# Kernel optimization log

Measured on AMD Instinct MI355X. Metric: run time of the kernel, lower is better.

Reference implementation:

```python
import jax, jax.numpy as jnp
from jax import lax
import numpy as np

B, C, H, W = 2, 256, 256, 256
NH, P = 8, 4
D = C // NH
EPS_BN = 1e-5
EPS_LN = 1e-5
EPS_ATT = 1e-6


def _maxpool(t):
    return lax.reduce_window(t, -jnp.inf, lax.max, (1, 1, P, P), (1, 1, P, P), 'VALID')


def _ln(t, g, b):  # t: [..., C]
    m = t.mean(-1, keepdims=True)
    v = ((t - m) ** 2).mean(-1, keepdims=True)
    return (t - m) * jax.lax.rsqrt(v + EPS_LN) * g + b


def _dw_bn(t, w, g, b, mu, var):  # depthwise 3x3 conv + BatchNorm2d (eval)
    y = lax.conv_general_dilated(t, w, (1, 1), ((1, 1), (1, 1)),
                                 dimension_numbers=('NCHW', 'OIHW', 'NCHW'),
                                 feature_group_count=C)
    s = g * jax.lax.rsqrt(var + EPS_BN)
    return y * s[None, :, None, None] + (b - mu * s)[None, :, None, None]


def _tokens(t, h, w):  # [N,(NH D),h,w] -> [N,(h w),NH,D]
    return t.reshape(-1, NH, D, h, w).transpose(0, 3, 4, 1, 2).reshape(-1, h * w, NH, D)


def setup_inputs() -> dict:
    key = jax.random.key(0)
    ks = jax.random.split(key, 16)
    inp = {
        'x': jax.random.normal(ks[0], (B, C, H, W), jnp.float32),
        'source': jax.random.normal(ks[1], (B, C, H, W), jnp.float32),
        'ln1_g': jnp.ones((C,), jnp.float32),
        'ln1_b': jnp.zeros((C,), jnp.float32),
        'merge_w': jax.random.normal(ks[2], (C, C), jnp.float32) * (1.0 / np.sqrt(C)),
        'mlp_w1': jax.random.normal(ks[3], (2 * C, 2 * C), jnp.float32) * (1.0 / np.sqrt(2 * C)),
        'mlp_w2': jax.random.normal(ks[4], (C, 2 * C), jnp.float32) * (1.0 / np.sqrt(2 * C)),
        'ln2_g': jnp.ones((C,), jnp.float32),
        'ln2_b': jnp.zeros((C,), jnp.float32),
    }
    for i, p in enumerate(['q', 'k', 'v']):
        kk = jax.random.split(ks[5 + i], 3)
        inp[p + '_w'] = jax.random.normal(kk[0], (C, 1, 3, 3), jnp.float32) * 0.2
        inp[p + '_bn_g'] = jnp.ones((C,), jnp.float32)
        inp[p + '_bn_b'] = jnp.zeros((C,), jnp.float32)
        inp[p + '_bn_m'] = jax.random.normal(kk[1], (C,), jnp.float32) * 0.05
        inp[p + '_bn_v'] = jax.random.uniform(kk[2], (C,), jnp.float32, 0.5, 1.5)
    return inp


def _forward(x, source, ln1_g, ln1_b,
             q_w, q_bn_g, q_bn_b, q_bn_m, q_bn_v,
             k_w, k_bn_g, k_bn_b, k_bn_m, k_bn_v,
             v_w, v_bn_g, v_bn_b, v_bn_m, v_bn_v,
             merge_w, mlp_w1, mlp_w2, ln2_g, ln2_b):
    h, w = H // P, W // P
    L = h * w
    # pre-norm after pooling (norm_before=True, max_pool path)
    q_sp = _ln(_maxpool(x).transpose(0, 2, 3, 1), ln1_g, ln1_b).transpose(0, 3, 1, 2)
    s_sp = _ln(_maxpool(source).transpose(0, 2, 3, 1), ln1_g, ln1_b).transpose(0, 3, 1, 2)
    # conv QKV projections (depthwise 3x3 + BN)
    q = _tokens(_dw_bn(q_sp, q_w, q_bn_g, q_bn_b, q_bn_m, q_bn_v), h, w)
    k = _tokens(_dw_bn(s_sp, k_w, k_bn_g, k_bn_b, k_bn_m, k_bn_v), h, w)
    v = _tokens(_dw_bn(s_sp, v_w, v_bn_g, v_bn_b, v_bn_m, v_bn_v), h, w)
    # LoFTR LinearAttention: feature map elu(x)+1
    Q = jax.nn.elu(q) + 1.0
    K = jax.nn.elu(k) + 1.0
    v_len = v.shape[1]
    KV = jnp.einsum('nshd,nshv->nhdv', K, v / v_len)
    Z = 1.0 / (jnp.einsum('nlhd,nhd->nlh', Q, K.sum(axis=1)) + EPS_ATT)
    msg = jnp.einsum('nlhd,nhdv,nlh->nlhv', Q, KV, Z) * v_len  # [N,L,NH,D]
    # merge + upsample
    msg = msg.reshape(B, L, C) @ merge_w.T
    msg = msg.reshape(B, h, w, C).transpose(0, 3, 1, 2)
    msg = jax.image.resize(msg, (B, C, H, W), method='bilinear')
    # merge-MLP + norm2 + residual
    cat = jnp.concatenate([x, msg], axis=1).transpose(0, 2, 3, 1)  # [B,H,W,2C]
    m = jax.nn.relu(cat @ mlp_w1.T) @ mlp_w2.T
    m = _ln(m, ln2_g, ln2_b).transpose(0, 3, 1, 2)
    return x + m


def reference(x, source, ln1_g, ln1_b,
              q_w, q_bn_g, q_bn_b, q_bn_m, q_bn_v,
              k_w, k_bn_g, k_bn_b, k_bn_m, k_bn_v,
              v_w, v_bn_g, v_bn_b, v_bn_m, v_bn_v,
              merge_w, mlp_w1, mlp_w2, ln2_g, ln2_b):
    return _forward(x, source, ln1_g, ln1_b,
                    q_w, q_bn_g, q_bn_b, q_bn_m, q_bn_v,
                    k_w, k_bn_g, k_bn_b, k_bn_m, k_bn_v,
                    v_w, v_bn_g, v_bn_b, v_bn_m, v_bn_v,
                    merge_w, mlp_w1, mlp_w2, ln2_g, ln2_b)
```

## Files before the change

kernel.cpp:

```cpp
#include <hip/hip_runtime.h>
#include <hip/hip_bf16.h>
#include <cstdint>


typedef __attribute__((ext_vector_type(8))) short bf16x8;
typedef __attribute__((ext_vector_type(4))) float f32x4;

#define SWZ(p, off) ((off) ^ (((p) & 7) << 4))

__device__ inline unsigned pk2bf(float a, float b) {
    unsigned ua = __builtin_bit_cast(unsigned, a);
    ua += 0x7fffu + ((ua >> 16) & 1u);
    unsigned ub = __builtin_bit_cast(unsigned, b);
    ub += 0x7fffu + ((ub >> 16) & 1u);
    return (ua >> 16) | (ub & 0xffff0000u);
}
__device__ inline float bitf(unsigned u) { return __builtin_bit_cast(float, u); }

__global__ void build_wimg(const float* __restrict__ w1, const float* __restrict__ w2,
                           uint4* __restrict__ w1img, uint4* __restrict__ w2img) {
    int idx = blockIdx.x * 256 + threadIdx.x;
    if (idx < 32768) {
        int rk = idx >> 11, jt = (idx >> 6) & 31, l = idx & 63;
        int j = jt * 16 + (l & 15);
        int k0 = rk * 32 + 8 * (l >> 4);
        const float* s = w1 + j * 512 + k0;
        uint4 pk;
        pk.x = pk2bf(s[0], s[1]); pk.y = pk2bf(s[2], s[3]);
        pk.z = pk2bf(s[4], s[5]); pk.w = pk2bf(s[6], s[7]);
        w1img[idx] = pk;
    } else {
        int id2 = idx - 32768;
        int rj = id2 >> 10, ct = (id2 >> 6) & 15, l = id2 & 63;
        int c = ct * 16 + (l & 15);
        int j0 = rj * 32 + 8 * (l >> 4);
        const float* s = w2 + c * 512 + j0;
        uint4 pk;
        pk.x = pk2bf(s[0], s[1]); pk.y = pk2bf(s[2], s[3]);
        pk.z = pk2bf(s[4], s[5]); pk.w = pk2bf(s[6], s[7]);
        w2img[id2] = pk;
    }
}

__global__ __launch_bounds__(512) void poolln_k(
    const float* __restrict__ x, const float* __restrict__ src,
    const float* __restrict__ g, const float* __restrict__ bvec,
    float* __restrict__ q_sp, float* __restrict__ s_sp) {
    __shared__ __align__(16) float tile[16640];
    __shared__ float ps[512];
    __shared__ float pq[512];
    __shared__ float mr[64];
    __shared__ float rr[64];
    int qy = blockIdx.x, b = blockIdx.y, z = blockIdx.z;
    const float* in = z ? src : x;
    float* out = z ? s_sp : q_sp;
    int t = threadIdx.x;
    int qx = t & 63;
    int gq = t >> 6;
    for (int cc = 0; cc < 32; cc++) {
        int cl = gq + cc * 8;
        const float* rp = in + (((b * 256 + cl) * 256) + 4 * qy) * 256 + 4 * qx;
        float4 r0 = *(const float4*)(rp);
        float4 r1 = *(const float4*)(rp + 256);
        float4 r2 = *(const float4*)(rp + 512);
        float4 r3 = *(const float4*)(rp + 768);
        float m = fmaxf(fmaxf(fmaxf(r0.x, r0.y), fmaxf(r0.z, r0.w)),
                        fmaxf(fmaxf(r1.x, r1.y), fmaxf(r1.z, r1.w)));
        m = fmaxf(m, fmaxf(fmaxf(r2.x, r2.y), fmaxf(r2.z, r2.w)));
        m = fmaxf(m, fmaxf(fmaxf(r3.x, r3.y), fmaxf(r3.z, r3.w)));
        tile[cl * 65 + qx] = m;
    }
    __syncthreads();
    {
        float s = 0.f, q = 0.f;
        for (int i = 0; i < 32; i++) {
            float v = tile[(gq * 32 + i) * 65 + qx];
            s += v; q += v * v;
        }
        ps[gq * 64 + qx] = s;
        pq[gq * 64 + qx] = q;
    }
    __syncthreads();
    if (t < 64) {
        float s = 0.f, q = 0.f;
#pragma unroll
        for (int ww = 0; ww < 8; ww++) { s += ps[ww * 64 + t]; q += pq[ww * 64 + t]; }
        float mean = s * (1.f / 256.f);
        float var = q * (1.f / 256.f) - mean * mean;
        mr[t] = mean; rr[t] = rsqrtf(var + 1e-5f);
    }
    __syncthreads();
    for (int cb4 = 0; cb4 < 4; cb4++) {
#pragma unroll
        for (int kk = 0; kk < 8; kk++) {
            int cl = t & 63;
            int qxx = gq + kk * 8;
            int c = cb4 * 64 + cl;
            float v = tile[c * 65 + qxx];
            out[((b * 64 + qy) * 64 + qxx) * 256 + c] =
                (v - mr[qxx]) * rr[qxx] * g[c] + bvec[c];
        }
    }
}

__global__ void dwconv_k(const float* __restrict__ q_sp, const float* __restrict__ s_sp,
                         const float* __restrict__ qw, const float* __restrict__ qg,
                         const float* __restrict__ qb, const float* __restrict__ qm,
                         const float* __restrict__ qvar,
                         const float* __restrict__ kw, const float* __restrict__ kg,
                         const float* __restrict__ kb, const float* __restrict__ km,
                         const float* __restrict__ kvar,
                         const float* __restrict__ vw, const float* __restrict__ vg,
                         const float* __restrict__ vb, const float* __restrict__ vm,
                         const float* __restrict__ vvar,
                         float* __restrict__ qf, float* __restrict__ kf, float* __restrict__ vf) {
    int bid = blockIdx.x;
    int b = bid >> 12, l = bid & 4095, y = l >> 6, xx = l & 63;
    int c = threadIdx.x;
    float aq = 0.f, ak = 0.f, av = 0.f;
#pragma unroll
    for (int ky = 0; ky < 3; ky++) {
        int yy = y + ky - 1;
        if (yy < 0 || yy > 63) continue;
#pragma unroll
        for (int kx = 0; kx < 3; kx++) {
            int x2 = xx + kx - 1;
            if (x2 < 0 || x2 > 63) continue;
            int off = ((b * 64 + yy) * 64 + x2) * 256 + c;
            float a = q_sp[off], s = s_sp[off];
            aq += a * qw[c * 9 + ky * 3 + kx];
            ak += s * kw[c * 9 + ky * 3 + kx];
            av += s * vw[c * 9 + ky * 3 + kx];
        }
    }
    float sq = qg[c] * rsqrtf(qvar[c] + 1e-5f);
    float sk = kg[c] * rsqrtf(kvar[c] + 1e-5f);
    float sv = vg[c] * rsqrtf(vvar[c] + 1e-5f);
    float oq = aq * sq + (qb[c] - qm[c] * sq);
    float ok = ak * sk + (kb[c] - km[c] * sk);
    float ov = av * sv + (vb[c] - vm[c] * sv);
    oq = oq > 0.f ? oq + 1.f : expm1f(oq) + 1.f;
    ok = ok > 0.f ? ok + 1.f : expm1f(ok) + 1.f;
    int o = (b * 4096 + l) * 256 + c;
    qf[o] = oq; kf[o] = ok; vf[o] = ov;
}

__global__ void kv_part(const float* __restrict__ kf, const float* __restrict__ vf,
                        float* __restrict__ kvp, float* __restrict__ kspart) {
    __shared__ float red[4][1024];
    __shared__ float kred[4][32];
    int bid = blockIdx.x;
    int bnh = bid >> 4, ch = bid & 15;
    int b = bnh >> 3, nh = bnh & 7;
    int t = threadIdx.x;
    int ls = t >> 6, dkg = (t >> 3) & 7, dvg = t & 7;
    const float* kb = kf + (size_t)b * 4096 * 256 + nh * 32 + dkg * 4;
    const float* vb = vf + (size_t)b * 4096 * 256 + nh * 32 + dvg * 4;
    int l0 = ch * 256 + ls * 64;
    float4 a0 = {0,0,0,0}, a1 = a0, a2 = a0, a3 = a0, ks = a0;
    for (int l = l0; l < l0 + 64; l++) {
        float4 k4 = *(const float4*)(kb + (size_t)l * 256);
        float4 v4 = *(const float4*)(vb + (size_t)l * 256);
        a0.x += k4.x * v4.x; a0.y += k4.x * v4.y; a0.z += k4.x * v4.z; a0.w += k4.x * v4.w;
        a1.x += k4.y * v4.x; a1.y += k4.y * v4.y; a1.z += k4.y * v4.z; a1.w += k4.y * v4.w;
        a2.x += k4.z * v4.x; a2.y += k4.z * v4.y; a2.z += k4.z * v4.z; a2.w += k4.z * v4.w;
        a3.x += k4.w * v4.x; a3.y += k4.w * v4.y; a3.z += k4.w * v4.z; a3.w += k4.w * v4.w;
        ks.x += k4.x; ks.y += k4.y; ks.z += k4.z; ks.w += k4.w;
    }
    int base = dkg * 128 + dvg * 4;
    *(float4*)(&red[ls][base])      = a0;
    *(float4*)(&red[ls][base + 32]) = a1;
    *(float4*)(&red[ls][base + 64]) = a2;
    *(float4*)(&red[ls][base + 96]) = a3;
    if (dvg == 0) *(float4*)(&kred[ls][dkg * 4]) = ks;
    __syncthreads();
    for (int e = t; e < 1024; e += 256)
        kvp[bid * 1024 + e] = red[0][e] + red[1][e] + red[2][e] + red[3][e];
    if (t < 32) kspart[bid * 32 + t] = kred[0][t] + kred[1][t] + kred[2][t] + kred[3][t];
}

__global__ void kv_red(const float* __restrict__ kvp, const float* __restrict__ kspart,
                       float* __restrict__ kv, float* __restrict__ ksum) {
    int bnh = blockIdx.x;
    int t = threadIdx.x;
    for (int e = t; e < 1024; e += 256) {
        float s = 0.f;
        for (int ch = 0; ch < 16; ch++) s += kvp[(bnh * 16 + ch) * 1024 + e];
        kv[bnh * 1024 + e] = s;
    }
    if (t < 32) {
        float s = 0.f;
        for (int ch = 0; ch < 16; ch++) s += kspart[(bnh * 16 + ch) * 32 + t];
        ksum[bnh * 32 + t] = s;
    }
}

__global__ void msgmerge_k(const float* __restrict__ qf, const float* __restrict__ kv,
                           const float* __restrict__ ksum, const float* __restrict__ mw,
                           float* __restrict__ merged) {
    __shared__ float Qs[8 * 256];
    __shared__ float Ms[8 * 256];
    int bid = blockIdx.x;
    int b = bid >> 9, l0 = (bid & 511) * 8;
    int t = threadIdx.x;
#pragma unroll
    for (int tt = 0; tt < 8; tt++) Qs[tt * 256 + t] = qf[(b * 4096 + l0 + tt) * 256 + t];
    __syncthreads();
    int nh = t >> 5, dv = t & 31;
    const float* kvb = kv + (b * 8 + nh) * 1024 + dv;
    const float* ksb = ksum + (b * 8 + nh) * 32;
    float sacc[8] = {0, 0, 0, 0, 0, 0, 0, 0};
    float zacc[8] = {0, 0, 0, 0, 0, 0, 0, 0};
    for (int dk = 0; dk < 32; dk++) {
        float kvv = kvb[dk * 32];
        float ksv = ksb[dk];
#pragma unroll
        for (int tt = 0; tt < 8; tt++) {
            float qv = Qs[tt * 256 + nh * 32 + dk];
            sacc[tt] += qv * kvv;
            zacc[tt] += qv * ksv;
        }
    }
#pragma unroll
    for (int tt = 0; tt < 8; tt++) Ms[tt * 256 + t] = sacc[tt] / (zacc[tt] + 1e-6f);
    __syncthreads();
    float acc8[8] = {0, 0, 0, 0, 0, 0, 0, 0};
    const float* wrow = mw + t * 256;
    for (int c = 0; c < 256; c++) {
        float wv = wrow[c];
#pragma unroll
        for (int tt = 0; tt < 8; tt++) acc8[tt] += Ms[tt * 256 + c] * wv;
    }
#pragma unroll
    for (int tt = 0; tt < 8; tt++) merged[(b * 4096 + l0 + tt) * 256 + t] = acc8[tt];
}

__global__ __launch_bounds__(1024) __attribute__((amdgpu_waves_per_eu(4))) void mlp_k(
    const float* __restrict__ x, const float* __restrict__ merged,
    const uint4* __restrict__ w1img, const uint4* __restrict__ w2img,
    const float* __restrict__ g2, const float* __restrict__ b2,
    float* __restrict__ out) {
    __shared__ __align__(16) char CATB[65536];
    __shared__ float ps[1024];
    __shared__ float pq[1024];
    __shared__ float mr[64];
    __shared__ float rr[64];
    __shared__ char lds_pad[12288];
    const int t = threadIdx.x;
    const int lane = t & 63;
    const int l15 = lane & 15, l4 = lane >> 4;
    const int w = t >> 6;
    const int X0 = blockIdx.x * 64;
    const int Y = blockIdx.y;
    const int b = blockIdx.z;
    if (g2 == nullptr) lds_pad[t] = 1;

    {
        const int p = lane;
        const int cg = w;
#pragma unroll
        for (int it = 0; it < 2; it++) {
            int c0 = cg * 16 + it * 8;
            float v[8];
#pragma unroll
            for (int j = 0; j < 8; j++)
                v[j] = x[((b * 256 + c0 + j) * 256 + Y) * 256 + X0 + p];
            uint4 pk;
            pk.x = pk2bf(v[0], v[1]); pk.y = pk2bf(v[2], v[3]);
            pk.z = pk2bf(v[4], v[5]); pk.w = pk2bf(v[6], v[7]);
            *(uint4*)(CATB + SWZ(p, p * 1024 + c0 * 2)) = pk;
        }
        float sy = (Y - 1.5f) * 0.25f;
        int iy0 = (int)floorf(sy);
        float fy = sy - (float)iy0;
        int y0c = iy0 < 0 ? 0 : iy0;
        int y1c = (iy0 + 1) > 63 ? 63 : (iy0 + 1);
        int X = X0 + p;
        float sx = (X - 1.5f) * 0.25f;
        int ix0 = (int)floorf(sx);
        float fx = sx - (float)ix0;
        int x0c = ix0 < 0 ? 0 : ix0;
        int x1c = (ix0 + 1) > 63 ? 63 : (ix0 + 1);
        float w00 = (1.f - fy) * (1.f - fx), w01 = (1.f - fy) * fx;
        float w10 = fy * (1.f - fx), w11 = fy * fx;
        const float* m00 = merged + ((b * 64 + y0c) * 64 + x0c) * 256;
        const float* m01 = merged + ((b * 64 + y0c) * 64 + x1c) * 256;
        const float* m10 = merged + ((b * 64 + y1c) * 64 + x0c) * 256;
        const float* m11 = merged + ((b * 64 + y1c) * 64 + x1c) * 256;
#pragma unroll
        for (int it = 0; it < 2; it++) {
            int c0 = cg * 16 + it * 8;
            float v[8];
#pragma unroll
            for (int j = 0; j < 8; j++)
                v[j] = w00 * m00[c0 + j] + w01 * m01[c0 + j] + w10 * m10[c0 + j] + w11 * m11[c0 + j];
            uint4 pk;
            pk.x = pk2bf(v[0], v[1]); pk.y = pk2bf(v[2], v[3]);
            pk.z = pk2bf(v[4], v[5]); pk.w = pk2bf(v[6], v[7]);
            *(uint4*)(CATB + SWZ(p, p * 1024 + (256 + c0) * 2)) = pk;
        }
    }
    __syncthreads();

    f32x4 acc[2][4];
#pragma unroll
    for (int a = 0; a < 2; a++)
#pragma unroll
        for (int n = 0; n < 4; n++) acc[a][n] = (f32x4){0.f, 0.f, 0.f, 0.f};
    {
        const uint4* w1p = w1img + (w * 2) * 64 + lane;
        for (int rk = 0; rk < 16; rk++) {
            bf16x8 wa[2];
#pragma unroll
            for (int a = 0; a < 2; a++) wa[a] = *(const bf16x8*)(w1p + rk * 2048 + a * 64);
#pragma unroll
            for (int n = 0; n < 4; n++) {
                int pr = n * 16 + l15;
                bf16x8 bfr = *(const bf16x8*)(CATB + SWZ(pr, pr * 1024 + rk * 64 + l4 * 16));
#pragma unroll
                for (int a = 0; a < 2; a++)
                    acc[a][n] = __builtin_amdgcn_mfma_f32_16x16x32_bf16(wa[a], bfr, acc[a][n], 0, 0, 0);
            }
        }
    }

    uint2 xs[4];
    {
        int c0 = w * 16 + l4 * 4;
#pragma unroll
        for (int n = 0; n < 4; n++) {
            int px = n * 16 + l15;
            xs[n] = *(const uint2*)(CATB + SWZ(px, px * 1024 + c0 * 2));
        }
    }
    __syncthreads();

#pragma unroll
    for (int a = 0; a < 2; a++) {
        int j0 = w * 32 + a * 16 + l4 * 4;
#pragma unroll
        for (int n = 0; n < 4; n++) {
            int pr = n * 16 + l15;
            uint2 u;
            u.x = pk2bf(fmaxf(acc[a][n][0], 0.f), fmaxf(acc[a][n][1], 0.f));
            u.y = pk2bf(fmaxf(acc[a][n][2], 0.f), fmaxf(acc[a][n][3], 0.f));
            *(uint2*)(CATB + SWZ(pr, pr * 1024 + j0 * 2)) = u;
        }
    }
    __syncthreads();

    f32x4 macc[4];
#pragma unroll
    for (int n = 0; n < 4; n++) macc[n] = (f32x4){0.f, 0.f, 0.f, 0.f};
    {
        const uint4* w2p = w2img + w * 64 + lane;
        for (int rj = 0; rj < 16; rj++) {
            bf16x8 va = *(const bf16x8*)(w2p + rj * 1024);
#pragma unroll
            for (int n = 0; n < 4; n++) {
                int pr = n * 16 + l15;
                bf16x8 bfr = *(const bf16x8*)(CATB + SWZ(pr, pr * 1024 + rj * 64 + l4 * 16));
                macc[n] = __builtin_amdgcn_mfma_f32_16x16x32_bf16(va, bfr, macc[n], 0, 0, 0);
            }
        }
    }

#pragma unroll
    for (int n = 0; n < 4; n++) {
        float ss = 0.f, qq = 0.f;
#pragma unroll
        for (int r = 0; r < 4; r++) { float vv = macc[n][r]; ss += vv; qq += vv * vv; }
        ss += __shfl_xor(ss, 16); ss += __shfl_xor(ss, 32);
        qq += __shfl_xor(qq, 16); qq += __shfl_xor(qq, 32);
        if (l4 == 0) {
            ps[w * 64 + n * 16 + l15] = ss;
            pq[w * 64 + n * 16 + l15] = qq;
        }
    }
    __syncthreads();
    if (t < 64) {
        float ss = 0.f, qq = 0.f;
#pragma unroll
        for (int ww = 0; ww < 16; ww++) {
            ss += ps[ww * 64 + t];
            qq += pq[ww * 64 + t];
        }
        float mean = ss * (1.f / 256.f);
        float var = qq * (1.f / 256.f) - mean * mean;
        mr[t] = mean; rr[t] = rsqrtf(var + 1e-5f);
    }
    __syncthreads();
    {
        int cbase = w * 16 + l4 * 4;
        float gg[4], bb[4];
#pragma unroll
        for (int r = 0; r < 4; r++) { gg[r] = g2[cbase + r]; bb[r] = b2[cbase + r]; }
#pragma unroll
        for (int n = 0; n < 4; n++) {
            int px = n * 16 + l15;
            uint2 u = xs[n];
            float xr[4];
            xr[0] = bitf(u.x << 16); xr[1] = bitf(u.x & 0xffff0000u);
            xr[2] = bitf(u.y << 16); xr[3] = bitf(u.y & 0xffff0000u);
            float mean = mr[px], rs = rr[px];
#pragma unroll
            for (int r = 0; r < 4; r++) {
                out[((b * 256 + cbase + r) * 256 + Y) * 256 + X0 + px] =
                    xr[r] + (macc[n][r] - mean) * rs * gg[r] + bb[r];
            }
        }
    }
}

extern "C" void kernel_launch(void* const* d_in, const int* in_sizes, int n_in,
                              void* d_out, int out_size, void* d_ws, size_t ws_size,
                              hipStream_t stream) {
    const float* x       = (const float*)d_in[0];
    const float* source  = (const float*)d_in[1];
    const float* ln1_g   = (const float*)d_in[2];
    const float* ln1_b   = (const float*)d_in[3];
    const float* merge_w = (const float*)d_in[4];
    const float* mlp_w1  = (const float*)d_in[5];
    const float* mlp_w2  = (const float*)d_in[6];
    const float* ln2_g   = (const float*)d_in[7];
    const float* ln2_b   = (const float*)d_in[8];
    const float* q_w = (const float*)d_in[9];
    const float* q_bn_g = (const float*)d_in[10];
    const float* q_bn_b = (const float*)d_in[11];
    const float* q_bn_m = (const float*)d_in[12];
    const float* q_bn_v = (const float*)d_in[13];
    const float* k_w = (const float*)d_in[14];
    const float* k_bn_g = (const float*)d_in[15];
    const float* k_bn_b = (const float*)d_in[16];
    const float* k_bn_m = (const float*)d_in[17];
    const float* k_bn_v = (const float*)d_in[18];
    const float* v_w = (const float*)d_in[19];
    const float* v_bn_g = (const float*)d_in[20];
    const float* v_bn_b = (const float*)d_in[21];
    const float* v_bn_m = (const float*)d_in[22];
    const float* v_bn_v = (const float*)d_in[23];
    float* out = (float*)d_out;

    float* ws = (float*)d_ws;
    float* q_sp   = ws + 0;
    float* s_sp   = ws + 2097152;
    float* qf     = ws + 4194304;
    float* kf     = ws + 6291456;
    float* vf     = ws + 8388608;
    float* merged = ws + 10485760;
    float* kvp    = ws + 0;
    float* kspart = ws + 262144;
    float* kv     = ws + 12650496;
    float* ksum   = ws + 12666880;
    uint4* w1img  = (uint4*)((char*)d_ws + 50669568);
    uint4* w2img  = (uint4*)((char*)d_ws + 51193856);

    build_wimg<<<192, 256, 0, stream>>>(mlp_w1, mlp_w2, w1img, w2img);
    poolln_k<<<dim3(64, 2, 2), 512, 0, stream>>>(x, source, ln1_g, ln1_b, q_sp, s_sp);
    dwconv_k<<<8192, 256, 0, stream>>>(q_sp, s_sp,
                                       q_w, q_bn_g, q_bn_b, q_bn_m, q_bn_v,
                                       k_w, k_bn_g, k_bn_b, k_bn_m, k_bn_v,
                                       v_w, v_bn_g, v_bn_b, v_bn_m, v_bn_v,
                                       qf, kf, vf);
    kv_part<<<256, 256, 0, stream>>>(kf, vf, kvp, kspart);
    kv_red<<<16, 256, 0, stream>>>(kvp, kspart, kv, ksum);
    msgmerge_k<<<1024, 256, 0, stream>>>(qf, kv, ksum, merge_w, merged);
    mlp_k<<<dim3(4, 256, 2), 1024, 0, stream>>>(x, merged, w1img, w2img, ln2_g, ln2_b, out);
}
```

Before: 336.5 us.

## Halve MLP block to 512 threads with larger per-wave MFMA tiles

The fused MLP kernel now runs 8 waves per block instead of 16. Each wave computes twice as many output rows, so every LDS B-fragment read feeds 4 (first GEMM) or 2 (second GEMM) MFMAs, which cuts LDS traffic per MFMA. The LDS padding array that capped occupancy is removed. The residual now rereads x from global memory in fp32 instead of keeping a bf16 copy in registers, which also changes numerics slightly. The cost is more accumulator registers per thread and fewer waves to hide latency.

```diff
diff --git a/kernel.cpp b/kernel.cpp
--- a/kernel.cpp
+++ b/kernel.cpp
@@ -235,17 +235,16 @@
     for (int tt = 0; tt < 8; tt++) merged[(b * 4096 + l0 + tt) * 256 + t] = acc8[tt];
 }
 
-__global__ __launch_bounds__(1024) __attribute__((amdgpu_waves_per_eu(4))) void mlp_k(
+__global__ __launch_bounds__(512) __attribute__((amdgpu_waves_per_eu(4))) void mlp_k(
     const float* __restrict__ x, const float* __restrict__ merged,
     const uint4* __restrict__ w1img, const uint4* __restrict__ w2img,
     const float* __restrict__ g2, const float* __restrict__ b2,
     float* __restrict__ out) {
     __shared__ __align__(16) char CATB[65536];
-    __shared__ float ps[1024];
-    __shared__ float pq[1024];
+    __shared__ float ps[512];
+    __shared__ float pq[512];
     __shared__ float mr[64];
     __shared__ float rr[64];
-    __shared__ char lds_pad[12288];
     const int t = threadIdx.x;
     const int lane = t & 63;
     const int l15 = lane & 15, l4 = lane >> 4;
@@ -253,14 +252,12 @@
     const int X0 = blockIdx.x * 64;
     const int Y = blockIdx.y;
     const int b = blockIdx.z;
-    if (g2 == nullptr) lds_pad[t] = 1;
 
     {
         const int p = lane;
-        const int cg = w;
-#pragma unroll
-        for (int it = 0; it < 2; it++) {
-            int c0 = cg * 16 + it * 8;
+#pragma unroll
+        for (int it = 0; it < 4; it++) {
+            int c0 = w * 32 + it * 8;
             float v[8];
 #pragma unroll
             for (int j = 0; j < 8; j++)
@@ -288,8 +285,8 @@
         const float* m10 = merged + ((b * 64 + y1c) * 64 + x0c) * 256;
         const float* m11 = merged + ((b * 64 + y1c) * 64 + x1c) * 256;
 #pragma unroll
-        for (int it = 0; it < 2; it++) {
-            int c0 = cg * 16 + it * 8;
+        for (int it = 0; it < 4; it++) {
+            int c0 = w * 32 + it * 8;
             float v[8];
 #pragma unroll
             for (int j = 0; j < 8; j++)
@@ -302,42 +299,34 @@
     }
     __syncthreads();
 
-    f32x4 acc[2][4];
-#pragma unroll
-    for (int a = 0; a < 2; a++)
+    f32x4 acc[4][4];
+#pragma unroll
+    for (int a = 0; a < 4; a++)
 #pragma unroll
         for (int n = 0; n < 4; n++) acc[a][n] = (f32x4){0.f, 0.f, 0.f, 0.f};
     {
-        const uint4* w1p = w1img + (w * 2) * 64 + lane;
+        const uint4* w1p = w1img + (w * 4) * 64 + lane;
         for (int rk = 0; rk < 16; rk++) {
-            bf16x8 wa[2];
-#pragma unroll
-            for (int a = 0; a < 2; a++) wa[a] = *(const bf16x8*)(w1p + rk * 2048 + a * 64);
+            bf16x8 bf[4];
 #pragma unroll
             for (int n = 0; n < 4; n++) {
                 int pr = n * 16 + l15;
-                bf16x8 bfr = *(const bf16x8*)(CATB + SWZ(pr, pr * 1024 + rk * 64 + l4 * 16));
-#pragma unroll
-                for (int a = 0; a < 2; a++)
-                    acc[a][n] = __builtin_amdgcn_mfma_f32_16x16x32_bf16(wa[a], bfr, acc[a][n], 0, 0, 0);
+                bf[n] = *(const bf16x8*)(CATB + SWZ(pr, pr * 1024 + rk * 64 + l4 * 16));
             }
-        }
-    }
-
-    uint2 xs[4];
-    {
-        int c0 = w * 16 + l4 * 4;
-#pragma unroll
-        for (int n = 0; n < 4; n++) {
-            int px = n * 16 + l15;
-            xs[n] = *(const uint2*)(CATB + SWZ(px, px * 1024 + c0 * 2));
-        }
-    }
-    __syncthreads();
-
-#pragma unroll
-    for (int a = 0; a < 2; a++) {
-        int j0 = w * 32 + a * 16 + l4 * 4;
+#pragma unroll
+            for (int a = 0; a < 4; a++) {
+                bf16x8 wa = *(const bf16x8*)(w1p + rk * 2048 + a * 64);
+#pragma unroll
+                for (int n = 0; n < 4; n++)
+                    acc[a][n] = __builtin_amdgcn_mfma_f32_16x16x32_bf16(wa, bf[n], acc[a][n], 0, 0, 0);
+            }
+        }
+    }
+    __syncthreads();
+
+#pragma unroll
+    for (int a = 0; a < 4; a++) {
+        int j0 = w * 64 + a * 16 + l4 * 4;
 #pragma unroll
         for (int n = 0; n < 4; n++) {
             int pr = n * 16 + l15;
@@ -349,18 +338,26 @@
     }
     __syncthreads();
 
-    f32x4 macc[4];
-#pragma unroll
-    for (int n = 0; n < 4; n++) macc[n] = (f32x4){0.f, 0.f, 0.f, 0.f};
+    f32x4 macc[2][4];
+#pragma unroll
+    for (int c = 0; c < 2; c++)
+#pragma unroll
+        for (int n = 0; n < 4; n++) macc[c][n] = (f32x4){0.f, 0.f, 0.f, 0.f};
     {
-        const uint4* w2p = w2img + w * 64 + lane;
+        const uint4* w2p = w2img + (w * 2) * 64 + lane;
         for (int rj = 0; rj < 16; rj++) {
-            bf16x8 va = *(const bf16x8*)(w2p + rj * 1024);
+            bf16x8 bf[4];
 #pragma unroll
             for (int n = 0; n < 4; n++) {
                 int pr = n * 16 + l15;
-                bf16x8 bfr = *(const bf16x8*)(CATB + SWZ(pr, pr * 1024 + rj * 64 + l4 * 16));
-                macc[n] = __builtin_amdgcn_mfma_f32_16x16x32_bf16(va, bfr, macc[n], 0, 0, 0);
+                bf[n] = *(const bf16x8*)(CATB + SWZ(pr, pr * 1024 + rj * 64 + l4 * 16));
+            }
+#pragma unroll
+            for (int c = 0; c < 2; c++) {
+                bf16x8 va = *(const bf16x8*)(w2p + rj * 1024 + c * 64);
+#pragma unroll
+                for (int n = 0; n < 4; n++)
+                    macc[c][n] = __builtin_amdgcn_mfma_f32_16x16x32_bf16(va, bf[n], macc[c][n], 0, 0, 0);
             }
         }
     }
@@ -369,7 +366,9 @@
     for (int n = 0; n < 4; n++) {
         float ss = 0.f, qq = 0.f;
 #pragma unroll
-        for (int r = 0; r < 4; r++) { float vv = macc[n][r]; ss += vv; qq += vv * vv; }
+        for (int c = 0; c < 2; c++)
+#pragma unroll
+            for (int r = 0; r < 4; r++) { float vv = macc[c][n][r]; ss += vv; qq += vv * vv; }
         ss += __shfl_xor(ss, 16); ss += __shfl_xor(ss, 32);
         qq += __shfl_xor(qq, 16); qq += __shfl_xor(qq, 32);
         if (l4 == 0) {
@@ -381,7 +380,7 @@
     if (t < 64) {
         float ss = 0.f, qq = 0.f;
 #pragma unroll
-        for (int ww = 0; ww < 16; ww++) {
+        for (int ww = 0; ww < 8; ww++) {
             ss += ps[ww * 64 + t];
             qq += pq[ww * 64 + t];
         }
@@ -390,23 +389,20 @@
         mr[t] = mean; rr[t] = rsqrtf(var + 1e-5f);
     }
     __syncthreads();
-    {
-        int cbase = w * 16 + l4 * 4;
+#pragma unroll
+    for (int cc = 0; cc < 2; cc++) {
+        int cbase = w * 32 + cc * 16 + l4 * 4;
         float gg[4], bb[4];
 #pragma unroll
         for (int r = 0; r < 4; r++) { gg[r] = g2[cbase + r]; bb[r] = b2[cbase + r]; }
 #pragma unroll
         for (int n = 0; n < 4; n++) {
             int px = n * 16 + l15;
-            uint2 u = xs[n];
-            float xr[4];
-            xr[0] = bitf(u.x << 16); xr[1] = bitf(u.x & 0xffff0000u);
-            xr[2] = bitf(u.y << 16); xr[3] = bitf(u.y & 0xffff0000u);
             float mean = mr[px], rs = rr[px];
 #pragma unroll
             for (int r = 0; r < 4; r++) {
-                out[((b * 256 + cbase + r) * 256 + Y) * 256 + X0 + px] =
-                    xr[r] + (macc[n][r] - mean) * rs * gg[r] + bb[r];
+                int off = ((b * 256 + cbase + r) * 256 + Y) * 256 + X0 + px;
+                out[off] = x[off] + (macc[cc][n][r] - mean) * rs * gg[r] + bb[r];
             }
         }
     }
@@ -465,5 +461,5 @@
     kv_part<<<256, 256, 0, stream>>>(kf, vf, kvp, kspart);
     kv_red<<<16, 256, 0, stream>>>(kvp, kspart, kv, ksum);
     msgmerge_k<<<1024, 256, 0, stream>>>(qf, kv, ksum, merge_w, merged);
-    mlp_k<<<dim3(4, 256, 2), 1024, 0, stream>>>(x, merged, w1img, w2img, ln2_g, ln2_b, out);
-}
+    mlp_k<<<dim3(4, 256, 2), 512, 0, stream>>>(x, merged, w1img, w2img, ln2_g, ln2_b, out);
+}
```

Measured after the change: 404.9 us. 1.2x slower.

## Double-buffer MLP weight tiles in LDS via global_load_lds

Applied to the files above, without the earlier changes.

The mlp_k kernel now copies each k-slice of the packed W1 and W2 weight images into a double-buffered LDS area (WBUF) with direct global-to-LDS loads, prefetching slice k+1 while computing on slice k. MFMA operands are then read from LDS instead of from per-wave global loads. This is meant to hide global/L2 latency on the weight stream. In exchange it adds a block-wide barrier every iteration of both GEMM loops and grows LDS use past the old padding. It also relies on the barrier covering completion of the asynchronous LDS DMA.

```diff
diff --git a/kernel.cpp b/kernel.cpp
--- a/kernel.cpp
+++ b/kernel.cpp
@@ -16,6 +16,12 @@
     return (ua >> 16) | (ub & 0xffff0000u);
 }
 __device__ inline float bitf(unsigned u) { return __builtin_bit_cast(float, u); }
+
+__device__ inline void gl_lds16(const void* g, void* l) {
+    __builtin_amdgcn_global_load_lds(
+        (const __attribute__((address_space(1))) void*)g,
+        (__attribute__((address_space(3))) void*)l, 16, 0, 0);
+}
 
 __global__ void build_wimg(const float* __restrict__ w1, const float* __restrict__ w2,
                            uint4* __restrict__ w1img, uint4* __restrict__ w2img) {
@@ -241,11 +247,11 @@
     const float* __restrict__ g2, const float* __restrict__ b2,
     float* __restrict__ out) {
     __shared__ __align__(16) char CATB[65536];
+    __shared__ __align__(16) uint4 WBUF[4096];
     __shared__ float ps[1024];
     __shared__ float pq[1024];
     __shared__ float mr[64];
     __shared__ float rr[64];
-    __shared__ char lds_pad[12288];
     const int t = threadIdx.x;
     const int lane = t & 63;
     const int l15 = lane & 15, l4 = lane >> 4;
@@ -253,7 +259,9 @@
     const int X0 = blockIdx.x * 64;
     const int Y = blockIdx.y;
     const int b = blockIdx.z;
-    if (g2 == nullptr) lds_pad[t] = 1;
+
+    gl_lds16(w1img + t, WBUF + t);
+    gl_lds16(w1img + 1024 + t, WBUF + 1024 + t);
 
     {
         const int p = lane;
@@ -307,21 +315,28 @@
     for (int a = 0; a < 2; a++)
 #pragma unroll
         for (int n = 0; n < 4; n++) acc[a][n] = (f32x4){0.f, 0.f, 0.f, 0.f};
-    {
-        const uint4* w1p = w1img + (w * 2) * 64 + lane;
-        for (int rk = 0; rk < 16; rk++) {
-            bf16x8 wa[2];
-#pragma unroll
-            for (int a = 0; a < 2; a++) wa[a] = *(const bf16x8*)(w1p + rk * 2048 + a * 64);
-#pragma unroll
-            for (int n = 0; n < 4; n++) {
-                int pr = n * 16 + l15;
-                bf16x8 bfr = *(const bf16x8*)(CATB + SWZ(pr, pr * 1024 + rk * 64 + l4 * 16));
-#pragma unroll
-                for (int a = 0; a < 2; a++)
-                    acc[a][n] = __builtin_amdgcn_mfma_f32_16x16x32_bf16(wa[a], bfr, acc[a][n], 0, 0, 0);
-            }
-        }
+    for (int rk = 0; rk < 16; rk++) {
+        if (rk < 15) {
+            const uint4* s = w1img + (rk + 1) * 2048;
+            uint4* d = WBUF + ((rk + 1) & 1) * 2048;
+            gl_lds16(s + t, d + t);
+            gl_lds16(s + 1024 + t, d + 1024 + t);
+        }
+        const uint4* wb = WBUF + (rk & 1) * 2048;
+        bf16x8 bf[4];
+#pragma unroll
+        for (int n = 0; n < 4; n++) {
+            int pr = n * 16 + l15;
+            bf[n] = *(const bf16x8*)(CATB + SWZ(pr, pr * 1024 + rk * 64 + l4 * 16));
+        }
+#pragma unroll
+        for (int a = 0; a < 2; a++) {
+            bf16x8 wa = *(const bf16x8*)(wb + (w * 2 + a) * 64 + lane);
+#pragma unroll
+            for (int n = 0; n < 4; n++)
+                acc[a][n] = __builtin_amdgcn_mfma_f32_16x16x32_bf16(wa, bf[n], acc[a][n], 0, 0, 0);
+        }
+        __syncthreads();
     }
 
     uint2 xs[4];
@@ -335,6 +350,7 @@
     }
     __syncthreads();
 
+    gl_lds16(w2img + t, WBUF + t);
 #pragma unroll
     for (int a = 0; a < 2; a++) {
         int j0 = w * 32 + a * 16 + l4 * 4;
@@ -352,17 +368,22 @@
     f32x4 macc[4];
 #pragma unroll
     for (int n = 0; n < 4; n++) macc[n] = (f32x4){0.f, 0.f, 0.f, 0.f};
-    {
-        const uint4* w2p = w2img + w * 64 + lane;
-        for (int rj = 0; rj < 16; rj++) {
-            bf16x8 va = *(const bf16x8*)(w2p + rj * 1024);
-#pragma unroll
-            for (int n = 0; n < 4; n++) {
-                int pr = n * 16 + l15;
-                bf16x8 bfr = *(const bf16x8*)(CATB + SWZ(pr, pr * 1024 + rj * 64 + l4 * 16));
-                macc[n] = __builtin_amdgcn_mfma_f32_16x16x32_bf16(va, bfr, macc[n], 0, 0, 0);
-            }
-        }
+    for (int rj = 0; rj < 16; rj++) {
+        if (rj < 15) {
+            gl_lds16(w2img + (rj + 1) * 1024 + t, WBUF + ((rj + 1) & 1) * 1024 + t);
+        }
+        const uint4* wb = WBUF + (rj & 1) * 1024;
+        bf16x8 bf[4];
+#pragma unroll
+        for (int n = 0; n < 4; n++) {
+            int pr = n * 16 + l15;
+            bf[n] = *(const bf16x8*)(CATB + SWZ(pr, pr * 1024 + rj * 64 + l4 * 16));
+        }
+        bf16x8 va = *(const bf16x8*)(wb + w * 64 + lane);
+#pragma unroll
+        for (int n = 0; n < 4; n++)
+            macc[n] = __builtin_amdgcn_mfma_f32_16x16x32_bf16(va, bf[n], macc[n], 0, 0, 0);
+        __syncthreads();
     }
 
 #pragma unroll
```

After: 415.4 us. 1.23x slower.

## Store intermediate activations as bf16 and regroup MFMA operand loads in MLP

Applied to the files above, without the earlier changes.

All intermediate buffers (pooled LN outputs, Q/K/V features, merged messages) are now stored as bf16 instead of fp32, halving the memory traffic between the small kernels. The MLP kernel drops an LDS padding array that was limiting occupancy, and loads all B fragments from LDS before issuing MFMAs to improve instruction-level overlap. The cost is reduced precision in intermediates, including K/V and the attention normalizer inputs.

```diff
diff --git a/kernel.cpp b/kernel.cpp
--- a/kernel.cpp
+++ b/kernel.cpp
@@ -5,6 +5,7 @@
 
 typedef __attribute__((ext_vector_type(8))) short bf16x8;
 typedef __attribute__((ext_vector_type(4))) float f32x4;
+typedef __attribute__((ext_vector_type(4))) unsigned short u16x4;
 
 #define SWZ(p, off) ((off) ^ (((p) & 7) << 4))
 
@@ -15,7 +16,17 @@
     ub += 0x7fffu + ((ub >> 16) & 1u);
     return (ua >> 16) | (ub & 0xffff0000u);
 }
+__device__ inline unsigned short bf16of(float a) {
+    unsigned ua = __builtin_bit_cast(unsigned, a);
+    ua += 0x7fffu + ((ua >> 16) & 1u);
+    return (unsigned short)(ua >> 16);
+}
 __device__ inline float bitf(unsigned u) { return __builtin_bit_cast(float, u); }
+__device__ inline float bf2f(unsigned short u) { return bitf(((unsigned)u) << 16); }
+__device__ inline float bfx(const uint4& v, int j) {
+    unsigned wdd = ((const unsigned*)&v)[j >> 1];
+    return (j & 1) ? bitf(wdd & 0xffff0000u) : bitf(wdd << 16);
+}
 
 __global__ void build_wimg(const float* __restrict__ w1, const float* __restrict__ w2,
                            uint4* __restrict__ w1img, uint4* __restrict__ w2img) {
@@ -45,7 +56,7 @@
 __global__ __launch_bounds__(512) void poolln_k(
     const float* __restrict__ x, const float* __restrict__ src,
     const float* __restrict__ g, const float* __restrict__ bvec,
-    float* __restrict__ q_sp, float* __restrict__ s_sp) {
+    unsigned short* __restrict__ q_sp, unsigned short* __restrict__ s_sp) {
     __shared__ __align__(16) float tile[16640];
     __shared__ float ps[512];
     __shared__ float pq[512];
@@ -53,7 +64,7 @@
     __shared__ float rr[64];
     int qy = blockIdx.x, b = blockIdx.y, z = blockIdx.z;
     const float* in = z ? src : x;
-    float* out = z ? s_sp : q_sp;
+    unsigned short* out = z ? s_sp : q_sp;
     int t = threadIdx.x;
     int qx = t & 63;
     int gq = t >> 6;
@@ -98,12 +109,12 @@
             int c = cb4 * 64 + cl;
             float v = tile[c * 65 + qxx];
             out[((b * 64 + qy) * 64 + qxx) * 256 + c] =
-                (v - mr[qxx]) * rr[qxx] * g[c] + bvec[c];
-        }
-    }
-}
-
-__global__ void dwconv_k(const float* __restrict__ q_sp, const float* __restrict__ s_sp,
+                bf16of((v - mr[qxx]) * rr[qxx] * g[c] + bvec[c]);
+        }
+    }
+}
+
+__global__ void dwconv_k(const unsigned short* __restrict__ q_sp, const unsigned short* __restrict__ s_sp,
                          const float* __restrict__ qw, const float* __restrict__ qg,
                          const float* __restrict__ qb, const float* __restrict__ qm,
                          const float* __restrict__ qvar,
@@ -113,7 +124,8 @@
                          const float* __restrict__ vw, const float* __restrict__ vg,
                          const float* __restrict__ vb, const float* __restrict__ vm,
                          const float* __restrict__ vvar,
-                         float* __restrict__ qf, float* __restrict__ kf, float* __restrict__ vf) {
+                         unsigned short* __restrict__ qf, unsigned short* __restrict__ kf,
+                         unsigned short* __restrict__ vf) {
     int bid = blockIdx.x;
     int b = bid >> 12, l = bid & 4095, y = l >> 6, xx = l & 63;
     int c = threadIdx.x;
@@ -127,7 +139,7 @@
             int x2 = xx + kx - 1;
             if (x2 < 0 || x2 > 63) continue;
             int off = ((b * 64 + yy) * 64 + x2) * 256 + c;
-            float a = q_sp[off], s = s_sp[off];
+            float a = bf2f(q_sp[off]), s = bf2f(s_sp[off]);
             aq += a * qw[c * 9 + ky * 3 + kx];
             ak += s * kw[c * 9 + ky * 3 + kx];
             av += s * vw[c * 9 + ky * 3 + kx];
@@ -142,10 +154,10 @@
     oq = oq > 0.f ? oq + 1.f : expm1f(oq) + 1.f;
     ok = ok > 0.f ? ok + 1.f : expm1f(ok) + 1.f;
     int o = (b * 4096 + l) * 256 + c;
-    qf[o] = oq; kf[o] = ok; vf[o] = ov;
-}
-
-__global__ void kv_part(const float* __restrict__ kf, const float* __restrict__ vf,
+    qf[o] = bf16of(oq); kf[o] = bf16of(ok); vf[o] = bf16of(ov);
+}
+
+__global__ void kv_part(const unsigned short* __restrict__ kf, const unsigned short* __restrict__ vf,
                         float* __restrict__ kvp, float* __restrict__ kspart) {
     __shared__ float red[4][1024];
     __shared__ float kred[4][32];
@@ -154,13 +166,15 @@
     int b = bnh >> 3, nh = bnh & 7;
     int t = threadIdx.x;
     int ls = t >> 6, dkg = (t >> 3) & 7, dvg = t & 7;
-    const float* kb = kf + (size_t)b * 4096 * 256 + nh * 32 + dkg * 4;
-    const float* vb = vf + (size_t)b * 4096 * 256 + nh * 32 + dvg * 4;
+    const unsigned short* kb = kf + (size_t)b * 4096 * 256 + nh * 32 + dkg * 4;
+    const unsigned short* vb = vf + (size_t)b * 4096 * 256 + nh * 32 + dvg * 4;
     int l0 = ch * 256 + ls * 64;
     float4 a0 = {0,0,0,0}, a1 = a0, a2 = a0, a3 = a0, ks = a0;
     for (int l = l0; l < l0 + 64; l++) {
-        float4 k4 = *(const float4*)(kb + (size_t)l * 256);
-        float4 v4 = *(const float4*)(vb + (size_t)l * 256);
+        u16x4 ku = *(const u16x4*)(kb + (size_t)l * 256);
+        u16x4 vu = *(const u16x4*)(vb + (size_t)l * 256);
+        float4 k4 = { bf2f(ku[0]), bf2f(ku[1]), bf2f(ku[2]), bf2f(ku[3]) };
+        float4 v4 = { bf2f(vu[0]), bf2f(vu[1]), bf2f(vu[2]), bf2f(vu[3]) };
         a0.x += k4.x * v4.x; a0.y += k4.x * v4.y; a0.z += k4.x * v4.z; a0.w += k4.x * v4.w;
         a1.x += k4.y * v4.x; a1.y += k4.y * v4.y; a1.z += k4.y * v4.z; a1.w += k4.y * v4.w;
         a2.x += k4.z * v4.x; a2.y += k4.z * v4.y; a2.z += k4.z * v4.z; a2.w += k4.z * v4.w;
@@ -195,16 +209,16 @@
     }
 }
 
-__global__ void msgmerge_k(const float* __restrict__ qf, const float* __restrict__ kv,
+__global__ void msgmerge_k(const unsigned short* __restrict__ qf, const float* __restrict__ kv,
                            const float* __restrict__ ksum, const float* __restrict__ mw,
-                           float* __restrict__ merged) {
+                           unsigned short* __restrict__ merged) {
     __shared__ float Qs[8 * 256];
     __shared__ float Ms[8 * 256];
     int bid = blockIdx.x;
     int b = bid >> 9, l0 = (bid & 511) * 8;
     int t = threadIdx.x;
 #pragma unroll
-    for (int tt = 0; tt < 8; tt++) Qs[tt * 256 + t] = qf[(b * 4096 + l0 + tt) * 256 + t];
+    for (int tt = 0; tt < 8; tt++) Qs[tt * 256 + t] = bf2f(qf[(b * 4096 + l0 + tt) * 256 + t]);
     __syncthreads();
     int nh = t >> 5, dv = t & 31;
     const float* kvb = kv + (b * 8 + nh) * 1024 + dv;
@@ -232,11 +246,11 @@
         for (int tt = 0; tt < 8; tt++) acc8[tt] += Ms[tt * 256 + c] * wv;
     }
 #pragma unroll
-    for (int tt = 0; tt < 8; tt++) merged[(b * 4096 + l0 + tt) * 256 + t] = acc8[tt];
+    for (int tt = 0; tt < 8; tt++) merged[(b * 4096 + l0 + tt) * 256 + t] = bf16of(acc8[tt]);
 }
 
 __global__ __launch_bounds__(1024) __attribute__((amdgpu_waves_per_eu(4))) void mlp_k(
-    const float* __restrict__ x, const float* __restrict__ merged,
+    const float* __restrict__ x, const unsigned short* __restrict__ merged,
     const uint4* __restrict__ w1img, const uint4* __restrict__ w2img,
     const float* __restrict__ g2, const float* __restrict__ b2,
     float* __restrict__ out) {
@@ -245,7 +259,6 @@
     __shared__ float pq[1024];
     __shared__ float mr[64];
     __shared__ float rr[64];
-    __shared__ char lds_pad[12288];
     const int t = threadIdx.x;
     const int lane = t & 63;
     const int l15 = lane & 15, l4 = lane >> 4;
@@ -253,7 +266,6 @@
     const int X0 = blockIdx.x * 64;
     const int Y = blockIdx.y;
     const int b = blockIdx.z;
-    if (g2 == nullptr) lds_pad[t] = 1;
 
     {
         const int p = lane;
@@ -283,17 +295,21 @@
         int x1c = (ix0 + 1) > 63 ? 63 : (ix0 + 1);
         float w00 = (1.f - fy) * (1.f - fx), w01 = (1.f - fy) * fx;
         float w10 = fy * (1.f - fx), w11 = fy * fx;
-        const float* m00 = merged + ((b * 64 + y0c) * 64 + x0c) * 256;
-        const float* m01 = merged + ((b * 64 + y0c) * 64 + x1c) * 256;
-        const float* m10 = merged + ((b * 64 + y1c) * 64 + x0c) * 256;
-        const float* m11 = merged + ((b * 64 + y1c) * 64 + x1c) * 256;
+        const unsigned short* m00 = merged + ((b * 64 + y0c) * 64 + x0c) * 256;
+        const unsigned short* m01 = merged + ((b * 64 + y0c) * 64 + x1c) * 256;
+        const unsigned short* m10 = merged + ((b * 64 + y1c) * 64 + x0c) * 256;
+        const unsigned short* m11 = merged + ((b * 64 + y1c) * 64 + x1c) * 256;
 #pragma unroll
         for (int it = 0; it < 2; it++) {
             int c0 = cg * 16 + it * 8;
+            uint4 a00 = *(const uint4*)(m00 + c0);
+            uint4 a01 = *(const uint4*)(m01 + c0);
+            uint4 a10 = *(const uint4*)(m10 + c0);
+            uint4 a11 = *(const uint4*)(m11 + c0);
             float v[8];
 #pragma unroll
             for (int j = 0; j < 8; j++)
-                v[j] = w00 * m00[c0 + j] + w01 * m01[c0 + j] + w10 * m10[c0 + j] + w11 * m11[c0 + j];
+                v[j] = w00 * bfx(a00, j) + w01 * bfx(a01, j) + w10 * bfx(a10, j) + w11 * bfx(a11, j);
             uint4 pk;
             pk.x = pk2bf(v[0], v[1]); pk.y = pk2bf(v[2], v[3]);
             pk.z = pk2bf(v[4], v[5]); pk.w = pk2bf(v[6], v[7]);
@@ -310,16 +326,18 @@
     {
         const uint4* w1p = w1img + (w * 2) * 64 + lane;
         for (int rk = 0; rk < 16; rk++) {
-            bf16x8 wa[2];
-#pragma unroll
-            for (int a = 0; a < 2; a++) wa[a] = *(const bf16x8*)(w1p + rk * 2048 + a * 64);
+            bf16x8 bf[4];
 #pragma unroll
             for (int n = 0; n < 4; n++) {
                 int pr = n * 16 + l15;
-                bf16x8 bfr = *(const bf16x8*)(CATB + SWZ(pr, pr * 1024 + rk * 64 + l4 * 16));
-#pragma unroll
-                for (int a = 0; a < 2; a++)
-                    acc[a][n] = __builtin_amdgcn_mfma_f32_16x16x32_bf16(wa[a], bfr, acc[a][n], 0, 0, 0);
+                bf[n] = *(const bf16x8*)(CATB + SWZ(pr, pr * 1024 + rk * 64 + l4 * 16));
+            }
+#pragma unroll
+            for (int a = 0; a < 2; a++) {
+                bf16x8 wa = *(const bf16x8*)(w1p + rk * 2048 + a * 64);
+#pragma unroll
+                for (int n = 0; n < 4; n++)
+                    acc[a][n] = __builtin_amdgcn_mfma_f32_16x16x32_bf16(wa, bf[n], acc[a][n], 0, 0, 0);
             }
         }
     }
@@ -355,13 +373,16 @@
     {
         const uint4* w2p = w2img + w * 64 + lane;
         for (int rj = 0; rj < 16; rj++) {
-            bf16x8 va = *(const bf16x8*)(w2p + rj * 1024);
+            bf16x8 bf[4];
 #pragma unroll
             for (int n = 0; n < 4; n++) {
                 int pr = n * 16 + l15;
-                bf16x8 bfr = *(const bf16x8*)(CATB + SWZ(pr, pr * 1024 + rj * 64 + l4 * 16));
-                macc[n] = __builtin_amdgcn_mfma_f32_16x16x32_bf16(va, bfr, macc[n], 0, 0, 0);
+                bf[n] = *(const bf16x8*)(CATB + SWZ(pr, pr * 1024 + rj * 64 + l4 * 16));
             }
+            bf16x8 va = *(const bf16x8*)(w2p + rj * 1024);
+#pragma unroll
+            for (int n = 0; n < 4; n++)
+                macc[n] = __builtin_amdgcn_mfma_f32_16x16x32_bf16(va, bf[n], macc[n], 0, 0, 0);
         }
     }
 
@@ -442,12 +463,12 @@
     float* out = (float*)d_out;
 
     float* ws = (float*)d_ws;
-    float* q_sp   = ws + 0;
-    float* s_sp   = ws + 2097152;
-    float* qf     = ws + 4194304;
-    float* kf     = ws + 6291456;
-    float* vf     = ws + 8388608;
-    float* merged = ws + 10485760;
+    unsigned short* q_sp   = (unsigned short*)(ws + 0);
+    unsigned short* s_sp   = (unsigned short*)(ws + 2097152);
+    unsigned short* qf     = (unsigned short*)(ws + 4194304);
+    unsigned short* kf     = (unsigned short*)(ws + 6291456);
+    unsigned short* vf     = (unsigned short*)(ws + 8388608);
+    unsigned short* merged = (unsigned short*)(ws + 10485760);
     float* kvp    = ws + 0;
     float* kspart = ws + 262144;
     float* kv     = ws + 12650496;
```

After: 373.2 us. 10.9% more time.
